# Kernel tuning notes

Hardware: AMD Instinct MI355X
Metric: run time of the kernel (lower is better)

The kernel has to match this reference:

```python
import jax, jax.numpy as jnp
import numpy as np

EPS = 1e-8  # torch cosine_similarity default eps


def setup_inputs() -> dict:
    key = jax.random.key(0)
    k1, k2, k3 = jax.random.split(key, 3)
    bsz, sent_len, cont_dim, mp_dim = 16, 512, 768, 20
    repres = jax.random.normal(k1, (bsz, sent_len, cont_dim), dtype=jnp.float32)
    max_att = jax.random.normal(k2, (bsz, sent_len, cont_dim), dtype=jnp.float32)
    # nn.Parameter initialized uniform_(-1, 1)
    weight = jax.random.uniform(k3, (mp_dim, cont_dim), dtype=jnp.float32, minval=-1.0, maxval=1.0)
    return {"repres": repres, "max_att": max_att, "weight": weight}


def reference(repres, max_att, weight):
    # Original math: a = repres[:,None,:] * w[None], b = max_att[:,None,:] * w[None]
    # cos = <a,b> / (max(||a||,eps) * max(||b||,eps)) along last dim.
    # Fused form: never materialize [N, mp_dim, cont_dim]; contract with w^2 directly.
    bsz, sent_len, cont_dim = repres.shape
    r = repres.reshape(-1, cont_dim)   # [N, D]
    m = max_att.reshape(-1, cont_dim)  # [N, D]
    w2 = weight * weight               # [P, D]
    dot = jnp.einsum('nd,pd->np', r * m, w2)              # [N, P]
    n1 = jnp.sqrt(jnp.einsum('nd,pd->np', r * r, w2))     # [N, P]
    n2 = jnp.sqrt(jnp.einsum('nd,pd->np', m * m, w2))     # [N, P]
    cos = dot / (jnp.maximum(n1, EPS) * jnp.maximum(n2, EPS))
    return cos.reshape(bsz, sent_len, weight.shape[0])
```

## Files before the change

kernel.cpp:

```cpp
#include <hip/hip_runtime.h>
#include <math.h>

static constexpr int D_DIM = 768;
static constexpr int NP    = 20;
static constexpr int NROWS = 8192;
static constexpr int ROWS_PER_BLOCK = 4;

template <int CTRL>
__device__ __forceinline__ float dpp_add(float x) {
  int t = __builtin_amdgcn_update_dpp(0, __float_as_int(x), CTRL, 0xF, 0xF, true);
  return x + __int_as_float(t);
}

__device__ __forceinline__ float wave_sum63(float x) {
  x = dpp_add<0x111>(x);
  x = dpp_add<0x112>(x);
  x = dpp_add<0x114>(x);
  x = dpp_add<0x118>(x);
  x = dpp_add<0x142>(x);
  x = dpp_add<0x143>(x);
  return x;
}

__global__ __launch_bounds__(256) void atte_cos_kernel(
    const float* __restrict__ repres,
    const float* __restrict__ max_att,
    const float* __restrict__ weight,
    float* __restrict__ out)
{
  const int tid  = threadIdx.x;
  const int wave = tid >> 6;
  const int lane = tid & 63;
  const int part = lane >> 4;
  const int sub  = lane & 15;
  const int d0    = part * 192 + sub * 4;
  const int pbase = wave * 5;

  float4 w2r[5][3];
#pragma unroll
  for (int p = 0; p < 5; ++p) {
#pragma unroll
    for (int k = 0; k < 3; ++k) {
      float4 w4 = *(const float4*)(weight + (pbase + p) * D_DIM + d0 + k * 64);
      w4.x *= w4.x; w4.y *= w4.y; w4.z *= w4.z; w4.w *= w4.w;
      w2r[p][k] = w4;
    }
  }

  const int row0 = blockIdx.x * ROWS_PER_BLOCK;

  float4 r4[3], m4[3];
  {
    const float* rp = repres  + (size_t)row0 * D_DIM + d0;
    const float* mp = max_att + (size_t)row0 * D_DIM + d0;
#pragma unroll
    for (int k = 0; k < 3; ++k) {
      r4[k] = *(const float4*)(rp + k * 64);
      m4[k] = *(const float4*)(mp + k * 64);
    }
  }

  for (int t = 0; t < ROWS_PER_BLOCK; ++t) {
    const int row = row0 + t;

    float prod[3][3][4];
#pragma unroll
    for (int k = 0; k < 3; ++k) {
      const float* rv_ = (const float*)&r4[k];
      const float* mv_ = (const float*)&m4[k];
#pragma unroll
      for (int c = 0; c < 4; ++c) {
        const float rv = rv_[c], mv = mv_[c];
        prod[k][0][c] = rv * mv;
        prod[k][1][c] = rv * rv;
        prod[k][2][c] = mv * mv;
      }
    }

    if (t + 1 < ROWS_PER_BLOCK) {
      const float* rp = repres  + (size_t)(row + 1) * D_DIM + d0;
      const float* mp = max_att + (size_t)(row + 1) * D_DIM + d0;
#pragma unroll
      for (int k = 0; k < 3; ++k) {
        r4[k] = *(const float4*)(rp + k * 64);
        m4[k] = *(const float4*)(mp + k * 64);
      }
    }

    float acc[15];
#pragma unroll
    for (int v = 0; v < 15; ++v) acc[v] = 0.0f;

#pragma unroll
    for (int k = 0; k < 3; ++k) {
#pragma unroll
      for (int p = 0; p < 5; ++p) {
        const float* w = (const float*)&w2r[p][k];
#pragma unroll
        for (int c = 0; c < 4; ++c) {
          acc[p*3+0] = fmaf(prod[k][0][c], w[c], acc[p*3+0]);
          acc[p*3+1] = fmaf(prod[k][1][c], w[c], acc[p*3+1]);
          acc[p*3+2] = fmaf(prod[k][2][c], w[c], acc[p*3+2]);
        }
      }
    }

#pragma unroll
    for (int v = 0; v < 15; ++v) acc[v] = wave_sum63(acc[v]);

    if (lane == 63) {
#pragma unroll
      for (int p = 0; p < 5; ++p) {
        const float dot = acc[p*3+0];
        const float n1  = fmaxf(sqrtf(acc[p*3+1]), 1e-8f);
        const float n2  = fmaxf(sqrtf(acc[p*3+2]), 1e-8f);
        out[(size_t)row * NP + pbase + p] = dot / (n1 * n2);
      }
    }
  }
}

extern "C" void kernel_launch(void* const* d_in, const int* in_sizes, int n_in,
                              void* d_out, int out_size, void* d_ws, size_t ws_size,
                              hipStream_t stream) {
  const float* repres  = (const float*)d_in[0];
  const float* max_att = (const float*)d_in[1];
  const float* weight  = (const float*)d_in[2];
  float* out = (float*)d_out;

  const int blocks = NROWS / ROWS_PER_BLOCK;
  atte_cos_kernel<<<blocks, 256, 0, stream>>>(repres, max_att, weight, out);
}
```

Before: 107.1 us.

## Stage row tiles into LDS via async global_load_lds, double rows per block

The kernel now bulk-loads 8 rows of repres and max_att for the whole block into shared memory with asynchronous global-to-LDS copies, issued before the weight-squared registers are built, so those loads overlap with weight setup. The per-row register prefetch is dropped. Rows per block go from 4 to 8, which halves the block count and amortizes the weight loads over more rows. The block uses 48KB of LDS and launch bounds of 3 blocks per SIMD, which may limit occupancy, and it drops the cross-row overlap the register prefetch used to give.

```diff
diff --git a/kernel.cpp b/kernel.cpp
--- a/kernel.cpp
+++ b/kernel.cpp
@@ -4,7 +4,8 @@
 static constexpr int D_DIM = 768;
 static constexpr int NP    = 20;
 static constexpr int NROWS = 8192;
-static constexpr int ROWS_PER_BLOCK = 4;
+static constexpr int RPB   = 8;
+static constexpr int BLOCKS = NROWS / RPB;
 
 template <int CTRL>
 __device__ __forceinline__ float dpp_add(float x) {
@@ -22,7 +23,14 @@
   return x;
 }
 
-__global__ __launch_bounds__(256) void atte_cos_kernel(
+__device__ __forceinline__ void async_copy16(const void* g, void* l) {
+  __builtin_amdgcn_global_load_lds(
+      (const __attribute__((address_space(1))) unsigned int*)(uintptr_t)g,
+      (__attribute__((address_space(3))) unsigned int*)(uint32_t)(uintptr_t)l,
+      16, 0, 0);
+}
+
+__global__ __launch_bounds__(256, 3) void atte_cos_kernel(
     const float* __restrict__ repres,
     const float* __restrict__ max_att,
     const float* __restrict__ weight,
@@ -36,6 +44,23 @@
   const int d0    = part * 192 + sub * 4;
   const int pbase = wave * 5;
 
+  __shared__ float lds[2 * RPB * D_DIM];
+
+  const int row0 = blockIdx.x * RPB;
+
+  {
+    const char* gr = (const char*)(repres  + (size_t)row0 * D_DIM);
+    const char* gm = (const char*)(max_att + (size_t)row0 * D_DIM);
+    char* lr = (char*)&lds[0];
+    char* lm = (char*)&lds[RPB * D_DIM];
+#pragma unroll
+    for (int c = 0; c < 6; ++c)
+      async_copy16(gr + c * 4096 + tid * 16, lr + c * 4096 + tid * 16);
+#pragma unroll
+    for (int c = 0; c < 6; ++c)
+      async_copy16(gm + c * 4096 + tid * 16, lm + c * 4096 + tid * 16);
+  }
+
   float4 w2r[5][3];
 #pragma unroll
   for (int p = 0; p < 5; ++p) {
@@ -47,44 +72,17 @@
     }
   }
 
-  const int row0 = blockIdx.x * ROWS_PER_BLOCK;
+  __syncthreads();
 
-  float4 r4[3], m4[3];
-  {
-    const float* rp = repres  + (size_t)row0 * D_DIM + d0;
-    const float* mp = max_att + (size_t)row0 * D_DIM + d0;
+  for (int t = 0; t < RPB; ++t) {
+    const float* lr = &lds[t * D_DIM + d0];
+    const float* lm = &lds[RPB * D_DIM + t * D_DIM + d0];
+
+    float4 r4[3], m4[3];
 #pragma unroll
     for (int k = 0; k < 3; ++k) {
-      r4[k] = *(const float4*)(rp + k * 64);
-      m4[k] = *(const float4*)(mp + k * 64);
-    }
-  }
-
-  for (int t = 0; t < ROWS_PER_BLOCK; ++t) {
-    const int row = row0 + t;
-
-    float prod[3][3][4];
-#pragma unroll
-    for (int k = 0; k < 3; ++k) {
-      const float* rv_ = (const float*)&r4[k];
-      const float* mv_ = (const float*)&m4[k];
-#pragma unroll
-      for (int c = 0; c < 4; ++c) {
-        const float rv = rv_[c], mv = mv_[c];
-        prod[k][0][c] = rv * mv;
-        prod[k][1][c] = rv * rv;
-        prod[k][2][c] = mv * mv;
-      }
-    }
-
-    if (t + 1 < ROWS_PER_BLOCK) {
-      const float* rp = repres  + (size_t)(row + 1) * D_DIM + d0;
-      const float* mp = max_att + (size_t)(row + 1) * D_DIM + d0;
-#pragma unroll
-      for (int k = 0; k < 3; ++k) {
-        r4[k] = *(const float4*)(rp + k * 64);
-        m4[k] = *(const float4*)(mp + k * 64);
-      }
+      r4[k] = *(const float4*)(lr + k * 64);
+      m4[k] = *(const float4*)(lm + k * 64);
     }
 
     float acc[15];
@@ -93,14 +91,22 @@
 
 #pragma unroll
     for (int k = 0; k < 3; ++k) {
+      float rmv[4], rrv[4], mmv[4];
+      const float* rv_ = (const float*)&r4[k];
+      const float* mv_ = (const float*)&m4[k];
+#pragma unroll
+      for (int c = 0; c < 4; ++c) {
+        const float rv = rv_[c], mv = mv_[c];
+        rmv[c] = rv * mv; rrv[c] = rv * rv; mmv[c] = mv * mv;
+      }
 #pragma unroll
       for (int p = 0; p < 5; ++p) {
         const float* w = (const float*)&w2r[p][k];
 #pragma unroll
         for (int c = 0; c < 4; ++c) {
-          acc[p*3+0] = fmaf(prod[k][0][c], w[c], acc[p*3+0]);
-          acc[p*3+1] = fmaf(prod[k][1][c], w[c], acc[p*3+1]);
-          acc[p*3+2] = fmaf(prod[k][2][c], w[c], acc[p*3+2]);
+          acc[p*3+0] = fmaf(rmv[c], w[c], acc[p*3+0]);
+          acc[p*3+1] = fmaf(rrv[c], w[c], acc[p*3+1]);
+          acc[p*3+2] = fmaf(mmv[c], w[c], acc[p*3+2]);
         }
       }
     }
@@ -114,7 +120,7 @@
         const float dot = acc[p*3+0];
         const float n1  = fmaxf(sqrtf(acc[p*3+1]), 1e-8f);
         const float n2  = fmaxf(sqrtf(acc[p*3+2]), 1e-8f);
-        out[(size_t)row * NP + pbase + p] = dot / (n1 * n2);
+        out[(size_t)(row0 + t) * NP + pbase + p] = dot / (n1 * n2);
       }
     }
   }
@@ -128,6 +134,5 @@
   const float* weight  = (const float*)d_in[2];
   float* out = (float*)d_out;
 
-  const int blocks = NROWS / ROWS_PER_BLOCK;
-  atte_cos_kernel<<<blocks, 256, 0, stream>>>(repres, max_att, weight, out);
+  atte_cos_kernel<<<BLOCKS, 256, 0, stream>>>(repres, max_att, weight, out);
 }
```

After: 110.5 us. 1.03x slower.
